# Performance work log

Hardware: AMD Instinct MI355X
Metric: run time of the kernel (lower is better)

## Reference

```python
import jax, jax.numpy as jnp
import numpy as np

D = 512          # embedding_dim (cfg.hidden_size)
K = 1024         # codebook_size
DECAY = 0.99
EPS = 1e-05
COMMITMENT_COST = 0.25


def setup_inputs() -> dict:
    key = jax.random.key(0)
    k1, k2, k3 = jax.random.split(key, 3)
    return {
        "inputs": jax.random.normal(k1, (32, 1024, D), dtype=jnp.float32),
        "embedding_weight": jax.random.normal(k2, (K, D), dtype=jnp.float32),
        "ema_cluster_size": jnp.zeros((K,), dtype=jnp.float32),
        "ema_w": jax.random.normal(k3, (K, D), dtype=jnp.float32),
    }


def reference(inputs, embedding_weight, ema_cluster_size, ema_w):
    input_shape = inputs.shape
    flat = inputs.reshape(-1, D)  # [N, D]

    # Squared L2 distances to every codebook entry: [N, K]
    distances = (
        jnp.sum(flat ** 2, axis=1, keepdims=True)
        + jnp.sum(embedding_weight ** 2, axis=1)
        - 2.0 * flat @ embedding_weight.T
    )
    idx = jnp.argmin(distances, axis=1)                      # [N]
    encodings = jax.nn.one_hot(idx, K, dtype=flat.dtype)     # [N, K]

    # ---- EMA codebook update (training path) ----
    counts = jnp.sum(encodings, axis=0)                      # == bincount(idx)
    new_cs = ema_cluster_size * DECAY + (1.0 - DECAY) * counts
    n = jnp.sum(new_cs)
    new_cs = (new_cs + EPS) / (n + K * EPS) * n              # Laplace smoothing
    # dw = encodings.T @ flat, done as a fused gather-reduce instead of dense matmul
    dw = jax.ops.segment_sum(flat, idx, num_segments=K)      # [K, D]
    new_ema_w = ema_w * DECAY + (1.0 - DECAY) * dw
    new_embedding = new_ema_w / new_cs[:, None]              # updated codebook

    # quantized = encodings @ new_embedding, expressed as a gather
    quantized = new_embedding[idx].reshape(input_shape)

    e_latent_loss = jnp.mean((jax.lax.stop_gradient(quantized) - inputs) ** 2)
    loss = COMMITMENT_COST * e_latent_loss

    # straight-through estimator
    quantized = inputs + jax.lax.stop_gradient(quantized - inputs)

    avg_probs = jnp.mean(encodings, axis=0)
    perplexity = jnp.exp(-jnp.sum(avg_probs * jnp.log(avg_probs + 1e-10)))
    return (loss, quantized, perplexity, encodings)
```

## Files before the change

### kernel.cpp

```cpp
#include <hip/hip_runtime.h>

#define NROWS 32768
#define DIM   512
#define KC    1024

typedef __attribute__((ext_vector_type(8)))  short short8v;
typedef __attribute__((ext_vector_type(16))) float f32x16;

#define AS1 __attribute__((address_space(1)))
#define AS3 __attribute__((address_space(3)))

__global__ __launch_bounds__(256) void k_enorm(const float* __restrict__ E,
                                               float* __restrict__ en2) {
    int w = threadIdx.x >> 6, lane = threadIdx.x & 63;
    int c = blockIdx.x * 4 + w;
    const float* row = E + (size_t)c * DIM;
    float4 a = *reinterpret_cast<const float4*>(&row[lane * 8]);
    float4 b = *reinterpret_cast<const float4*>(&row[lane * 8 + 4]);
    float s = a.x*a.x + a.y*a.y + a.z*a.z + a.w*a.w
            + b.x*b.x + b.y*b.y + b.z*b.z + b.w*b.w;
    #pragma unroll
    for (int off = 32; off; off >>= 1) s += __shfl_xor(s, off);
    if (!lane) en2[c] = s;
}

__device__ __forceinline__ void split_bf16(float v, short& hi, short& lo) {
    unsigned u = __float_as_uint(v);
    unsigned r = u + 0x7FFFu + ((u >> 16) & 1u);
    hi = (short)(r >> 16);
    float hif = __uint_as_float(r & 0xFFFF0000u);
    float rem = v - hif;
    unsigned u2 = __float_as_uint(rem);
    unsigned r2 = u2 + 0x7FFFu + ((u2 >> 16) & 1u);
    lo = (short)(r2 >> 16);
}

__device__ __forceinline__ unsigned long long pack_key(float d, int c) {
    unsigned u = __float_as_uint(d);
    u = (u & 0x80000000u) ? ~u : (u | 0x80000000u);
    return ((unsigned long long)u << 32) | (unsigned)c;
}

__global__ __launch_bounds__(256) void k_split(const float* __restrict__ x,
                                               const float* __restrict__ E,
                                               short* __restrict__ xfrag,
                                               short* __restrict__ efrag) {
    __shared__ short hbuf[32][520];
    __shared__ short lbuf[32][520];
    int b = blockIdx.x, t = threadIdx.x;
    const float* src;
    short* dst;
    if (b < NROWS / 32) {
        src = x + (size_t)b * 32 * DIM;
        dst = xfrag + (size_t)b * 32768;
    } else {
        src = E + (size_t)(b - NROWS / 32) * 32 * DIM;
        dst = efrag + (size_t)(b - NROWS / 32) * 32768;
    }
    #pragma unroll
    for (int f = 0; f < 16; ++f) {
        int u = t + f * 256;
        int row = u >> 7, c4 = (u & 127) * 4;
        float4 v = *reinterpret_cast<const float4*>(&src[row * DIM + c4]);
        short4 h4, l4;
        split_bf16(v.x, h4.x, l4.x); split_bf16(v.y, h4.y, l4.y);
        split_bf16(v.z, h4.z, l4.z); split_bf16(v.w, h4.w, l4.w);
        *reinterpret_cast<short4*>(&hbuf[row][c4]) = h4;
        *reinterpret_cast<short4*>(&lbuf[row][c4]) = l4;
    }
    __syncthreads();
    #pragma unroll
    for (int f = 0; f < 16; ++f) {
        int u = t + f * 256;
        int lane = u & 63, h = (u >> 6) & 1, kb = u >> 7;
        int row = lane & 31, k0 = kb * 16 + (lane >> 5) * 8;
        const short* s = h ? &lbuf[row][k0] : &hbuf[row][k0];
        short8v val = *reinterpret_cast<const short8v*>(s);
        *reinterpret_cast<short8v*>(&dst[(size_t)u * 8]) = val;
    }
}

__global__ __launch_bounds__(256, 2) void k_argmin(const short* __restrict__ xfrag,
                                                   const short* __restrict__ efrag,
                                                   const float* __restrict__ en2,
                                                   unsigned long long* __restrict__ packed) {
    __shared__ short sbuf[3][12288];
    const int tid = threadIdx.x;
    const int w = tid >> 6, l = tid & 63;
    const int wr = w >> 1, wc = w & 1;
    const int l31 = l & 31, lh = l >> 5;

    int bid = blockIdx.x;
    int xcd = bid & 7, j = bid >> 3;
    int row0 = (xcd * 32 + (j >> 2)) * 128;
    int c0   = (j & 3) * 256;

    const short* gsrc[6];
    #pragma unroll
    for (int s = 0; s < 6; ++s) {
        int q = s * 4 + w, g = q >> 1, h = q & 1;
        const short* base = (g < 4)
            ? xfrag + (size_t)(row0 / 32 + g) * 32768
            : efrag + (size_t)(c0 / 32 + (g - 4)) * 32768;
        gsrc[s] = base + h * 512 + l * 8;
    }

    f32x16 acc[2][4];
    #pragma unroll
    for (int a = 0; a < 2; ++a)
        #pragma unroll
        for (int b = 0; b < 4; ++b)
            #pragma unroll
            for (int r = 0; r < 16; ++r) acc[a][b][r] = 0.f;

    #pragma unroll
    for (int s = 0; s < 6; ++s)
        __builtin_amdgcn_global_load_lds((const AS1 void*)gsrc[s],
                                         (AS3 void*)&sbuf[0][(s * 4 + w) * 512],
                                         16, 0, 0);
    #pragma unroll
    for (int s = 0; s < 6; ++s)
        __builtin_amdgcn_global_load_lds((const AS1 void*)(gsrc[s] + 1024),
                                         (AS3 void*)&sbuf[1][(s * 4 + w) * 512],
                                         16, 0, 0);
    asm volatile("s_waitcnt vmcnt(6)" ::: "memory");
    __builtin_amdgcn_s_barrier();
    __builtin_amdgcn_sched_barrier(0);

    #pragma unroll 3
    for (int kb = 0; kb < 30; ++kb) {
        const int cur = kb % 3, nxt = (kb + 2) % 3;
        #pragma unroll
        for (int s = 0; s < 6; ++s)
            __builtin_amdgcn_global_load_lds(
                (const AS1 void*)(gsrc[s] + (size_t)(kb + 2) * 1024),
                (AS3 void*)&sbuf[nxt][(s * 4 + w) * 512], 16, 0, 0);
        {
            short8v ah[2], al[2], bh[4], bl[4];
            const short* sb = sbuf[cur];
            #pragma unroll
            for (int m = 0; m < 2; ++m) {
                int g = wr * 2 + m;
                ah[m] = *reinterpret_cast<const short8v*>(&sb[(g * 2 + 0) * 512 + l * 8]);
                al[m] = *reinterpret_cast<const short8v*>(&sb[(g * 2 + 1) * 512 + l * 8]);
            }
            #pragma unroll
            for (int n = 0; n < 4; ++n) {
                int g = 4 + wc * 4 + n;
                bh[n] = *reinterpret_cast<const short8v*>(&sb[(g * 2 + 0) * 512 + l * 8]);
                bl[n] = *reinterpret_cast<const short8v*>(&sb[(g * 2 + 1) * 512 + l * 8]);
            }
            #pragma unroll
            for (int m = 0; m < 2; ++m)
                #pragma unroll
                for (int n = 0; n < 4; ++n) {
                    acc[m][n] = __builtin_amdgcn_mfma_f32_32x32x16_bf16(
                        ah[m], bh[n], acc[m][n], 0, 0, 0);
                    acc[m][n] = __builtin_amdgcn_mfma_f32_32x32x16_bf16(
                        ah[m], bl[n], acc[m][n], 0, 0, 0);
                    acc[m][n] = __builtin_amdgcn_mfma_f32_32x32x16_bf16(
                        al[m], bh[n], acc[m][n], 0, 0, 0);
                }
        }
        asm volatile("s_waitcnt vmcnt(6) lgkmcnt(0)" ::: "memory");
        __builtin_amdgcn_s_barrier();
        __builtin_amdgcn_sched_barrier(0);
    }

    #pragma unroll
    for (int e = 0; e < 2; ++e) {
        const int kb = 30 + e, cur = kb % 3;
        short8v ah[2], al[2], bh[4], bl[4];
        const short* sb = sbuf[cur];
        #pragma unroll
        for (int m = 0; m < 2; ++m) {
            int g = wr * 2 + m;
            ah[m] = *reinterpret_cast<const short8v*>(&sb[(g * 2 + 0) * 512 + l * 8]);
            al[m] = *reinterpret_cast<const short8v*>(&sb[(g * 2 + 1) * 512 + l * 8]);
        }
        #pragma unroll
        for (int n = 0; n < 4; ++n) {
            int g = 4 + wc * 4 + n;
            bh[n] = *reinterpret_cast<const short8v*>(&sb[(g * 2 + 0) * 512 + l * 8]);
            bl[n] = *reinterpret_cast<const short8v*>(&sb[(g * 2 + 1) * 512 + l * 8]);
        }
        #pragma unroll
        for (int m = 0; m < 2; ++m)
            #pragma unroll
            for (int n = 0; n < 4; ++n) {
                acc[m][n] = __builtin_amdgcn_mfma_f32_32x32x16_bf16(
                    ah[m], bh[n], acc[m][n], 0, 0, 0);
                acc[m][n] = __builtin_amdgcn_mfma_f32_32x32x16_bf16(
                    ah[m], bl[n], acc[m][n], 0, 0, 0);
                acc[m][n] = __builtin_amdgcn_mfma_f32_32x32x16_bf16(
                    al[m], bh[n], acc[m][n], 0, 0, 0);
            }
        if (e == 0) {
            asm volatile("s_waitcnt vmcnt(0) lgkmcnt(0)" ::: "memory");
            __builtin_amdgcn_s_barrier();
            __builtin_amdgcn_sched_barrier(0);
        }
    }

    float e2[4];
    #pragma unroll
    for (int n = 0; n < 4; ++n) e2[n] = en2[c0 + wc * 128 + n * 32 + l31];
    #pragma unroll
    for (int m = 0; m < 2; ++m) {
        #pragma unroll
        for (int r = 0; r < 16; ++r) {
            unsigned long long key = 0xFFFFFFFFFFFFFFFFull;
            #pragma unroll
            for (int n = 0; n < 4; ++n) {
                float d = fmaf(-2.f, acc[m][n][r], e2[n]);
                unsigned long long k = pack_key(d, c0 + wc * 128 + n * 32 + l31);
                if (k < key) key = k;
            }
            #pragma unroll
            for (int off = 1; off < 32; off <<= 1) {
                unsigned long long o = __shfl_xor(key, off);
                if (o < key) key = o;
            }
            if (l31 == 0) {
                int grow = row0 + wr * 64 + m * 32 + (r & 3) + 8 * (r >> 2) + 4 * lh;
                atomicMin(&packed[grow], key);
            }
        }
    }
}

__global__ __launch_bounds__(256) void k_hist(const unsigned long long* __restrict__ packed,
                                              int* __restrict__ idx,
                                              int* __restrict__ counts) {
    __shared__ int h[KC];
    for (int i = threadIdx.x; i < KC; i += 256) h[i] = 0;
    __syncthreads();
    int g = blockIdx.x * 256 + threadIdx.x;
    int c = (int)(unsigned)(packed[g] & 0xFFFFFFFFull);
    idx[g] = c;
    atomicAdd(&h[c], 1);
    __syncthreads();
    for (int i = threadIdx.x; i < KC; i += 256)
        if (h[i]) atomicAdd(&counts[i], h[i]);
}

__global__ __launch_bounds__(1024) void k_meta(const int* __restrict__ counts,
                                               const float* __restrict__ ema_cs,
                                               float* __restrict__ smoothed,
                                               int* __restrict__ offsets,
                                               int* __restrict__ cursor,
                                               float* __restrict__ perp_out) {
    __shared__ float red[KC];
    __shared__ int sc[KC];
    int t = threadIdx.x;
    int cnt = counts[t];
    float cs = ema_cs[t] * 0.99f + 0.01f * (float)cnt;
    red[t] = cs; __syncthreads();
    for (int s = 512; s; s >>= 1) { if (t < s) red[t] += red[t + s]; __syncthreads(); }
    float n = red[0];
    __syncthreads();
    float sm = (cs + 1e-5f) / (n + 1024.f * 1e-5f) * n;
    smoothed[t] = sm;
    float p = (float)cnt / 32768.f;
    red[t] = p * logf(p + 1e-10f);
    __syncthreads();
    for (int s = 512; s; s >>= 1) { if (t < s) red[t] += red[t + s]; __syncthreads(); }
    if (!t) perp_out[0] = expf(-red[0]);
    sc[t] = cnt; __syncthreads();
    for (int s = 1; s < KC; s <<= 1) {
        int v = (t >= s) ? sc[t - s] : 0;
        __syncthreads();
        sc[t] += v;
        __syncthreads();
    }
    int off = sc[t] - cnt;
    offsets[t] = off;
    cursor[t] = off;
}

__global__ __launch_bounds__(256) void k_scatter(const int* __restrict__ idx,
                                                 int* __restrict__ cursor,
                                                 int* __restrict__ bucket) {
    int g = blockIdx.x * 256 + threadIdx.x;
    int c = idx[g];
    int pos = atomicAdd(&cursor[c], 1);
    bucket[pos] = g;
}

__global__ __launch_bounds__(256) void k_dw(const float* __restrict__ x,
                                            const float* __restrict__ ema_w,
                                            const int* __restrict__ offsets,
                                            const int* __restrict__ counts,
                                            const int* __restrict__ bucket,
                                            const float* __restrict__ smoothed,
                                            float* __restrict__ newE) {
    __shared__ int rows[256];
    int k = blockIdx.x, t = threadIdx.x;
    int beg = offsets[k], m = counts[k];
    float a0 = 0.f, a1 = 0.f;
    for (int base = 0; base < m; base += 256) {
        int n = min(256, m - base);
        __syncthreads();
        if (t < n) rows[t] = bucket[beg + base + t];
        __syncthreads();
        int i = 0;
        for (; i + 4 <= n; i += 4) {
            int r0 = rows[i], r1 = rows[i + 1], r2 = rows[i + 2], r3 = rows[i + 3];
            float v00 = x[(size_t)r0 * DIM + t];
            float v01 = x[(size_t)r0 * DIM + t + 256];
            float v10 = x[(size_t)r1 * DIM + t];
            float v11 = x[(size_t)r1 * DIM + t + 256];
            float v20 = x[(size_t)r2 * DIM + t];
            float v21 = x[(size_t)r2 * DIM + t + 256];
            float v30 = x[(size_t)r3 * DIM + t];
            float v31 = x[(size_t)r3 * DIM + t + 256];
            a0 += v00 + v10 + v20 + v30;
            a1 += v01 + v11 + v21 + v31;
        }
        for (; i < n; ++i) {
            int r = rows[i];
            a0 += x[(size_t)r * DIM + t];
            a1 += x[(size_t)r * DIM + t + 256];
        }
    }
    float sm = smoothed[k];
    newE[(size_t)k * DIM + t]       = (ema_w[(size_t)k * DIM + t]       * 0.99f + 0.01f * a0) / sm;
    newE[(size_t)k * DIM + t + 256] = (ema_w[(size_t)k * DIM + t + 256] * 0.99f + 0.01f * a1) / sm;
}

__global__ __launch_bounds__(256) void k_qe(const float* __restrict__ x,
                                            const int* __restrict__ idx,
                                            const float* __restrict__ newE,
                                            float* __restrict__ outq,
                                            float* __restrict__ enc,
                                            float* __restrict__ partials) {
    int b = blockIdx.x, t = threadIdx.x;
    int row8 = b * 8;
    float lp = 0.f;
    #pragma unroll
    for (int it = 0; it < 4; ++it) {
        int slot = t + it * 256;
        int r = slot >> 7;
        int c4 = (slot & 127) * 4;
        int row = row8 + r;
        int code = idx[row];
        float4 in = *reinterpret_cast<const float4*>(&x[(size_t)row * DIM + c4]);
        float4 q  = *reinterpret_cast<const float4*>(&newE[(size_t)code * DIM + c4]);
        float4 d;
        d.x = q.x - in.x; d.y = q.y - in.y; d.z = q.z - in.z; d.w = q.w - in.w;
        float4 o;
        o.x = in.x + d.x; o.y = in.y + d.y; o.z = in.z + d.z; o.w = in.w + d.w;
        *reinterpret_cast<float4*>(&outq[(size_t)row * DIM + c4]) = o;
        lp += d.x*d.x + d.y*d.y + d.z*d.z + d.w*d.w;
    }
    {
        int er = row8 + (t >> 5);
        int l32 = t & 31;
        int one = idx[er];
        float4* dst = reinterpret_cast<float4*>(enc + (size_t)er * KC);
        #pragma unroll
        for (int s = 0; s < 8; ++s) {
            int c4 = l32 + s * 32;
            int base = c4 * 4;
            float4 v;
            v.x = (one == base)     ? 1.f : 0.f;
            v.y = (one == base + 1) ? 1.f : 0.f;
            v.z = (one == base + 2) ? 1.f : 0.f;
            v.w = (one == base + 3) ? 1.f : 0.f;
            dst[c4] = v;
        }
    }
    #pragma unroll
    for (int off = 32; off; off >>= 1) lp += __shfl_xor(lp, off);
    __shared__ float wr[4];
    int lane = t & 63, w = t >> 6;
    if (!lane) wr[w] = lp;
    __syncthreads();
    if (t == 0) partials[b] = wr[0] + wr[1] + wr[2] + wr[3];
}

__global__ __launch_bounds__(256) void k_lossfin(const float* __restrict__ partials,
                                                 float* __restrict__ out0) {
    __shared__ double red[256];
    double s = 0.0;
    for (int i = threadIdx.x; i < 4096; i += 256) s += (double)partials[i];
    red[threadIdx.x] = s; __syncthreads();
    for (int st = 128; st; st >>= 1) {
        if (threadIdx.x < st) red[threadIdx.x] += red[threadIdx.x + st];
        __syncthreads();
    }
    if (!threadIdx.x) out0[0] = (float)(0.25 * red[0] / 16777216.0);
}

extern "C" void kernel_launch(void* const* d_in, const int* in_sizes, int n_in,
                              void* d_out, int out_size, void* d_ws, size_t ws_size,
                              hipStream_t stream) {
    const float* x   = (const float*)d_in[0];
    const float* E   = (const float*)d_in[1];
    const float* ecs = (const float*)d_in[2];
    const float* emw = (const float*)d_in[3];
    float* out = (float*)d_out;

    char* ws = (char*)d_ws;
    int*   idx      = (int*)(ws + 0);
    int*   bucket   = (int*)(ws + 131072);
    float* en2      = (float*)(ws + 262144);
    int*   counts   = (int*)(ws + 266240);
    int*   offsets  = (int*)(ws + 270336);
    int*   cursor   = (int*)(ws + 274432);
    float* smoothed = (float*)(ws + 278528);
    float* newE     = (float*)(ws + 282624);
    float* partials = (float*)(ws + 282624 + 2097152);
    unsigned long long* packed = (unsigned long long*)newE;

    float* out_loss = out;
    float* out_q    = out + 1;
    float* out_perp = out + 16777217;
    float* out_enc  = out + 16777218;

    short* xfrag = (short*)out_enc;
    short* efrag = xfrag + (size_t)NROWS * DIM * 2;

    hipMemsetAsync(counts, 0, KC * sizeof(int), stream);
    hipMemsetAsync(packed, 0xFF, NROWS * sizeof(unsigned long long), stream);

    k_enorm  <<<KC / 4, 256, 0, stream>>>(E, en2);
    k_split  <<<NROWS / 32 + KC / 32, 256, 0, stream>>>(x, E, xfrag, efrag);
    k_argmin <<<(NROWS / 128) * 4, 256, 0, stream>>>(xfrag, efrag, en2, packed);
    k_hist   <<<NROWS / 256, 256, 0, stream>>>(packed, idx, counts);
    k_meta   <<<1, 1024, 0, stream>>>(counts, ecs, smoothed, offsets, cursor, out_perp);
    k_scatter<<<NROWS / 256, 256, 0, stream>>>(idx, cursor, bucket);
    k_dw     <<<KC, 256, 0, stream>>>(x, emw, offsets, counts, bucket, smoothed, newE);
    k_qe     <<<NROWS / 8, 256, 0, stream>>>(x, idx, newE, out_q, out_enc, partials);
    k_lossfin<<<1, 256, 0, stream>>>(partials, out_loss);
}
```

Baseline: 310.0 us.

## Fold memsets into split kernel, warp-shuffle meta, split dw grid, drop sched barriers

Moves the counts zeroing and the packed-key 0xFF fill into k_split, so two memset launches disappear. k_meta replaces its shared-memory tree reductions and scan with wave shuffles plus a small cross-wave pass. k_dw gets twice as many blocks, each accumulating half of the dimensions, which raises parallelism for the gather-reduce. The sched_barrier hints in the argmin main loop are removed, letting the compiler interleave across the barriers.

Measured after the change: 301.1 us. 1.03x faster.

```diff
diff --git a/kernel.cpp b/kernel.cpp
--- a/kernel.cpp
+++ b/kernel.cpp
@@ -44,7 +44,9 @@
 __global__ __launch_bounds__(256) void k_split(const float* __restrict__ x,
                                                const float* __restrict__ E,
                                                short* __restrict__ xfrag,
-                                               short* __restrict__ efrag) {
+                                               short* __restrict__ efrag,
+                                               int* __restrict__ counts,
+                                               unsigned long long* __restrict__ packed) {
     __shared__ short hbuf[32][520];
     __shared__ short lbuf[32][520];
     int b = blockIdx.x, t = threadIdx.x;
@@ -53,9 +55,17 @@
     if (b < NROWS / 32) {
         src = x + (size_t)b * 32 * DIM;
         dst = xfrag + (size_t)b * 32768;
+        if (b == 0) {
+            #pragma unroll
+            for (int i = 0; i < 4; ++i) counts[t + i * 256] = 0;
+        }
     } else {
-        src = E + (size_t)(b - NROWS / 32) * 32 * DIM;
-        dst = efrag + (size_t)(b - NROWS / 32) * 32768;
+        int eb = b - NROWS / 32;
+        src = E + (size_t)eb * 32 * DIM;
+        dst = efrag + (size_t)eb * 32768;
+        unsigned long long* p = packed + eb * 1024;
+        #pragma unroll
+        for (int i = 0; i < 4; ++i) p[t + i * 256] = 0xFFFFFFFFFFFFFFFFull;
     }
     #pragma unroll
     for (int f = 0; f < 16; ++f) {
@@ -125,7 +135,6 @@
                                          16, 0, 0);
     asm volatile("s_waitcnt vmcnt(6)" ::: "memory");
     __builtin_amdgcn_s_barrier();
-    __builtin_amdgcn_sched_barrier(0);
 
     #pragma unroll 3
     for (int kb = 0; kb < 30; ++kb) {
@@ -164,7 +173,6 @@
         }
         asm volatile("s_waitcnt vmcnt(6) lgkmcnt(0)" ::: "memory");
         __builtin_amdgcn_s_barrier();
-        __builtin_amdgcn_sched_barrier(0);
     }
 
     #pragma unroll
@@ -198,7 +206,6 @@
         if (e == 0) {
             asm volatile("s_waitcnt vmcnt(0) lgkmcnt(0)" ::: "memory");
             __builtin_amdgcn_s_barrier();
-            __builtin_amdgcn_sched_barrier(0);
         }
     }
 
@@ -250,32 +257,42 @@
                                                int* __restrict__ offsets,
                                                int* __restrict__ cursor,
                                                float* __restrict__ perp_out) {
-    __shared__ float red[KC];
-    __shared__ int sc[KC];
-    int t = threadIdx.x;
+    __shared__ float ws1[16], ws2[16];
+    __shared__ int wsum[16];
+    int t = threadIdx.x, lane = t & 63, w = t >> 6;
     int cnt = counts[t];
     float cs = ema_cs[t] * 0.99f + 0.01f * (float)cnt;
-    red[t] = cs; __syncthreads();
-    for (int s = 512; s; s >>= 1) { if (t < s) red[t] += red[t + s]; __syncthreads(); }
-    float n = red[0];
+    float p = (float)cnt / 32768.f;
+    float v1 = cs, v2 = p * logf(p + 1e-10f);
+    #pragma unroll
+    for (int off = 32; off; off >>= 1) {
+        v1 += __shfl_xor(v1, off);
+        v2 += __shfl_xor(v2, off);
+    }
+    int s = cnt;
+    #pragma unroll
+    for (int off = 1; off < 64; off <<= 1) {
+        int u = __shfl_up(s, off);
+        if (lane >= off) s += u;
+    }
+    if (lane == 0) { ws1[w] = v1; ws2[w] = v2; }
+    if (lane == 63) wsum[w] = s;
     __syncthreads();
-    float sm = (cs + 1e-5f) / (n + 1024.f * 1e-5f) * n;
-    smoothed[t] = sm;
-    float p = (float)cnt / 32768.f;
-    red[t] = p * logf(p + 1e-10f);
-    __syncthreads();
-    for (int s = 512; s; s >>= 1) { if (t < s) red[t] += red[t + s]; __syncthreads(); }
-    if (!t) perp_out[0] = expf(-red[0]);
-    sc[t] = cnt; __syncthreads();
-    for (int s = 1; s < KC; s <<= 1) {
-        int v = (t >= s) ? sc[t - s] : 0;
-        __syncthreads();
-        sc[t] += v;
-        __syncthreads();
-    }
-    int off = sc[t] - cnt;
-    offsets[t] = off;
-    cursor[t] = off;
+    float n = 0.f;
+    #pragma unroll
+    for (int i = 0; i < 16; ++i) n += ws1[i];
+    smoothed[t] = (cs + 1e-5f) / (n + 1024.f * 1e-5f) * n;
+    if (t == 0) {
+        float sp = 0.f;
+        #pragma unroll
+        for (int i = 0; i < 16; ++i) sp += ws2[i];
+        perp_out[0] = expf(-sp);
+    }
+    int wo = 0;
+    for (int i = 0; i < 16; ++i) if (i < w) wo += wsum[i];
+    int off_ = wo + s - cnt;
+    offsets[t] = off_;
+    cursor[t] = off_;
 }
 
 __global__ __launch_bounds__(256) void k_scatter(const int* __restrict__ idx,
@@ -295,9 +312,10 @@
                                             const float* __restrict__ smoothed,
                                             float* __restrict__ newE) {
     __shared__ int rows[256];
-    int k = blockIdx.x, t = threadIdx.x;
+    int k = blockIdx.x >> 1, half = blockIdx.x & 1, t = threadIdx.x;
+    int d = half * 256 + t;
     int beg = offsets[k], m = counts[k];
-    float a0 = 0.f, a1 = 0.f;
+    float a = 0.f;
     for (int base = 0; base < m; base += 256) {
         int n = min(256, m - base);
         __syncthreads();
@@ -305,27 +323,16 @@
         __syncthreads();
         int i = 0;
         for (; i + 4 <= n; i += 4) {
-            int r0 = rows[i], r1 = rows[i + 1], r2 = rows[i + 2], r3 = rows[i + 3];
-            float v00 = x[(size_t)r0 * DIM + t];
-            float v01 = x[(size_t)r0 * DIM + t + 256];
-            float v10 = x[(size_t)r1 * DIM + t];
-            float v11 = x[(size_t)r1 * DIM + t + 256];
-            float v20 = x[(size_t)r2 * DIM + t];
-            float v21 = x[(size_t)r2 * DIM + t + 256];
-            float v30 = x[(size_t)r3 * DIM + t];
-            float v31 = x[(size_t)r3 * DIM + t + 256];
-            a0 += v00 + v10 + v20 + v30;
-            a1 += v01 + v11 + v21 + v31;
-        }
-        for (; i < n; ++i) {
-            int r = rows[i];
-            a0 += x[(size_t)r * DIM + t];
-            a1 += x[(size_t)r * DIM + t + 256];
-        }
-    }
-    float sm = smoothed[k];
-    newE[(size_t)k * DIM + t]       = (ema_w[(size_t)k * DIM + t]       * 0.99f + 0.01f * a0) / sm;
-    newE[(size_t)k * DIM + t + 256] = (ema_w[(size_t)k * DIM + t + 256] * 0.99f + 0.01f * a1) / sm;
+            float v0 = x[(size_t)rows[i]     * DIM + d];
+            float v1 = x[(size_t)rows[i + 1] * DIM + d];
+            float v2 = x[(size_t)rows[i + 2] * DIM + d];
+            float v3 = x[(size_t)rows[i + 3] * DIM + d];
+            a += v0 + v1 + v2 + v3;
+        }
+        for (; i < n; ++i) a += x[(size_t)rows[i] * DIM + d];
+    }
+    newE[(size_t)k * DIM + d] =
+        (ema_w[(size_t)k * DIM + d] * 0.99f + 0.01f * a) / smoothed[k];
 }
 
 __global__ __launch_bounds__(256) void k_qe(const float* __restrict__ x,
@@ -421,16 +428,14 @@
     short* xfrag = (short*)out_enc;
     short* efrag = xfrag + (size_t)NROWS * DIM * 2;
 
-    hipMemsetAsync(counts, 0, KC * sizeof(int), stream);
-    hipMemsetAsync(packed, 0xFF, NROWS * sizeof(unsigned long long), stream);
-
     k_enorm  <<<KC / 4, 256, 0, stream>>>(E, en2);
-    k_split  <<<NROWS / 32 + KC / 32, 256, 0, stream>>>(x, E, xfrag, efrag);
+    k_split  <<<NROWS / 32 + KC / 32, 256, 0, stream>>>(x, E, xfrag, efrag,
+                                                        counts, packed);
     k_argmin <<<(NROWS / 128) * 4, 256, 0, stream>>>(xfrag, efrag, en2, packed);
     k_hist   <<<NROWS / 256, 256, 0, stream>>>(packed, idx, counts);
     k_meta   <<<1, 1024, 0, stream>>>(counts, ecs, smoothed, offsets, cursor, out_perp);
     k_scatter<<<NROWS / 256, 256, 0, stream>>>(idx, cursor, bucket);
-    k_dw     <<<KC, 256, 0, stream>>>(x, emw, offsets, counts, bucket, smoothed, newE);
+    k_dw     <<<KC * 2, 256, 0, stream>>>(x, emw, offsets, counts, bucket, smoothed, newE);
     k_qe     <<<NROWS / 8, 256, 0, stream>>>(x, idx, newE, out_q, out_enc, partials);
     k_lossfin<<<1, 256, 0, stream>>>(partials, out_loss);
 }
```
